# Performance work log

Hardware: AMD Instinct MI355X
Metric: run time of the kernel (lower is better)

## Reference

```python
import jax, jax.numpy as jnp
import numpy as np

E = 1024      # embed_dim
H = 16        # num_heads
HD = E // H   # head_dim = 64
M = 64        # num_landmarks


def setup_inputs() -> dict:
    key = jax.random.key(0)
    ks = jax.random.split(key, 9)
    B, Lq, Lk = 2, 2048, 2048
    inv = 1.0 / np.sqrt(E)
    return {
        "query": jax.random.normal(ks[0], (B, Lq, E), dtype=jnp.float32),
        "key":   jax.random.normal(ks[1], (B, Lk, E), dtype=jnp.float32),
        "value": jax.random.normal(ks[2], (B, Lk, E), dtype=jnp.float32),
        # learned params (xavier-ish scale)
        "Wv": jax.random.normal(ks[3], (E, E), dtype=jnp.float32) * inv,
        "bv": jnp.zeros((E,), dtype=jnp.float32),
        "Wl": jax.random.normal(ks[4], (M, E), dtype=jnp.float32) * inv,
        "bl": jnp.zeros((M,), dtype=jnp.float32),
        "Wo": jax.random.normal(ks[5], (E, E), dtype=jnp.float32) * inv,
        "bo": jnp.zeros((E,), dtype=jnp.float32),
    }


def reference(query, key, value, Wv, bv, Wl, bl, Wo, bo):
    B, Lq, _ = query.shape
    Lk = key.shape[1]
    # value projection -> [B, H, Lk, HD]
    v = (value @ Wv.T + bv).reshape(B, Lk, H, HD).transpose(0, 2, 1, 3)
    # landmark projections + softmax over landmark dim
    ql = jax.nn.softmax((query @ Wl.T + bl) / np.sqrt(M), axis=-1)  # [B, Lq, M]
    kl = jax.nn.softmax((key @ Wl.T + bl) / np.sqrt(M), axis=-1)    # [B, Lk, M]
    # landmark attention: [B, Lq, Lk], scaled by sqrt(head_dim), softmax over keys
    attn = jax.nn.softmax(
        jnp.einsum("bqm,bkm->bqk", ql, kl) / np.sqrt(HD), axis=-1)
    # apply shared attention across heads: [B, H, Lq, HD]
    out_h = jnp.einsum("bqk,bhkd->bhqd", attn, v)
    out = out_h.transpose(0, 2, 1, 3).reshape(B, Lq, E)
    return out @ Wo.T + bo
```

## Files before the change

### kernel.cpp

```cpp
#include <hip/hip_runtime.h>
#include <hip/hip_bf16.h>
#include <cstdint>

typedef unsigned short u16;
typedef __attribute__((ext_vector_type(8))) short short8;
typedef __attribute__((ext_vector_type(4))) float f32x4;
typedef __attribute__((ext_vector_type(4))) unsigned short us4;

__device__ __forceinline__ u16 f2bf(float f) {
    union { float f; unsigned int i; } v; v.f = f;
    unsigned int x = v.i;
    unsigned int r = x + 0x7fffu + ((x >> 16) & 1u);
    return (u16)(r >> 16);
}

enum { EPI_F32 = 0, EPI_BF16 = 1, EPI_EXP_RS = 3, EPI_F32_DIV_CB = 4, EPI_LMSM = 5 };

template <int BM, int BN, int EPI>
__global__ void __launch_bounds__(256)
gemm_bt(const u16* __restrict__ A, const u16* __restrict__ B, void* __restrict__ Cv,
        int M, int N, int K, long sA, long sB, long sC,
        const float* __restrict__ biasCol, float* __restrict__ rowScale, float expScale)
{
    constexpr int BK = 64;
    constexpr int MFRAG = (BM + 31) / 32;
    constexpr int NFRAG = BN / 32;
    __shared__ alignas(16) u16 As[BM * BK];
    __shared__ alignas(16) u16 Bs[BN * BK];

    const int tid = threadIdx.x;
    const int lane = tid & 63;
    const int quad = lane >> 4;
    const int l15 = lane & 15;
    const int w = tid >> 6;
    const int wm = w >> 1, wn = w & 1;
    const int z = blockIdx.z;
    const int m0 = blockIdx.y * BM;
    const int n0 = blockIdx.x * BN;

    const u16* Ab = A + (long)z * sA + (long)m0 * K;
    const u16* Bb = B + (long)z * sB + (long)n0 * K;

    const int r8 = tid >> 3;
    const int cl = tid & 7;
    const int cg = ((cl ^ (r8 & 7)) * 8);

    const u16* ap[(BM + 31) / 32];
#pragma unroll
    for (int j = 0; j < (BM + 31) / 32; ++j) ap[j] = Ab + (long)(j * 32 + r8) * K + cg;
    const u16* bp[BN / 32];
#pragma unroll
    for (int j = 0; j < BN / 32; ++j) bp[j] = Bb + (long)(j * 32 + r8) * K + cg;

    f32x4 acc[MFRAG][NFRAG] = {};

    const int sw = l15 & 7;

    for (int k0 = 0; k0 < K; k0 += BK) {
#pragma unroll
        for (int j = 0; j < (BM + 31) / 32; ++j) {
            __builtin_amdgcn_global_load_lds(
                (const __attribute__((address_space(1))) void*)(ap[j]),
                (__attribute__((address_space(3))) void*)(&As[(j * 32 + r8) * BK + cl * 8]),
                16, 0, 0);
            ap[j] += BK;
        }
#pragma unroll
        for (int j = 0; j < BN / 32; ++j) {
            __builtin_amdgcn_global_load_lds(
                (const __attribute__((address_space(1))) void*)(bp[j]),
                (__attribute__((address_space(3))) void*)(&Bs[(j * 32 + r8) * BK + cl * 8]),
                16, 0, 0);
            bp[j] += BK;
        }
        __syncthreads();
#pragma unroll
        for (int ks = 0; ks < 2; ++ks) {
            short8 af[MFRAG], bfr[NFRAG];
#pragma unroll
            for (int i = 0; i < MFRAG; ++i)
                af[i] = *(const short8*)&As[(wm * (BM / 2) + i * 16 + l15) * BK +
                                            (((ks * 4 + quad) ^ sw) * 8)];
#pragma unroll
            for (int i = 0; i < NFRAG; ++i)
                bfr[i] = *(const short8*)&Bs[(wn * (BN / 2) + i * 16 + l15) * BK +
                                             (((ks * 4 + quad) ^ sw) * 8)];
#pragma unroll
            for (int i = 0; i < MFRAG; ++i)
#pragma unroll
                for (int jn = 0; jn < NFRAG; ++jn)
                    acc[i][jn] = __builtin_amdgcn_mfma_f32_16x16x32_bf16(af[i], bfr[jn], acc[i][jn], 0, 0, 0);
        }
        __syncthreads();
    }

    if constexpr (EPI == EPI_LMSM) {
        __shared__ float red[2][BM];
        float ev[4][NFRAG];
#pragma unroll
        for (int r = 0; r < 4; ++r) {
            float s = 0.f;
#pragma unroll
            for (int jn = 0; jn < NFRAG; ++jn) {
                const int col = wn * (BN / 2) + jn * 16 + l15;
                float v = exp2f((acc[0][jn][r] + biasCol[col]) * expScale);
                ev[r][jn] = v; s += v;
            }
            s += __shfl_xor(s, 1); s += __shfl_xor(s, 2);
            s += __shfl_xor(s, 4); s += __shfl_xor(s, 8);
            if (l15 == 0) red[wn][wm * 16 + quad * 4 + r] = s;
        }
        __syncthreads();
#pragma unroll
        for (int r = 0; r < 4; ++r) {
            const int mrow = wm * 16 + quad * 4 + r;
            const float inv = 1.0f / (red[0][mrow] + red[1][mrow]);
            const long m = m0 + mrow;
#pragma unroll
            for (int jn = 0; jn < NFRAG; ++jn) {
                const int col = wn * (BN / 2) + jn * 16 + l15;
                ((u16*)Cv)[m * N + col] = f2bf(ev[r][jn] * inv);
            }
        }
        return;
    } else {
#pragma unroll
        for (int i = 0; i < MFRAG; ++i) {
            const int mb = m0 + wm * (BM / 2) + i * 16 + quad * 4;
#pragma unroll
            for (int r = 0; r < 4; ++r) {
                const int m = mb + r;
                float rin = 0.f;
                if constexpr (EPI == EPI_F32_DIV_CB) rin = 1.0f / rowScale[(long)z * M + m];
                float rowsum = 0.f;
#pragma unroll
                for (int jn = 0; jn < NFRAG; ++jn) {
                    const int col = n0 + wn * (BN / 2) + jn * 16 + l15;
                    float v = acc[i][jn][r];
                    if constexpr (EPI == EPI_EXP_RS) { v = exp2f(v * expScale); rowsum += v; }
                    if constexpr (EPI == EPI_F32_DIV_CB) v = v * rin + biasCol[col];
                    if constexpr (EPI == EPI_F32 || EPI == EPI_F32_DIV_CB)
                        ((float*)Cv)[(long)z * sC + (long)m * N + col] = v;
                    else
                        ((u16*)Cv)[(long)z * sC + (long)m * N + col] = f2bf(v);
                }
                if constexpr (EPI == EPI_EXP_RS) {
                    rowsum += __shfl_xor(rowsum, 1);
                    rowsum += __shfl_xor(rowsum, 2);
                    rowsum += __shfl_xor(rowsum, 4);
                    rowsum += __shfl_xor(rowsum, 8);
                    if (l15 == 0) atomicAdd(&rowScale[(long)z * M + m], rowsum);
                }
            }
        }
    }
}

__global__ void __launch_bounds__(256)
cast_qkv(const float* __restrict__ a, const float* __restrict__ b, const float* __restrict__ c,
         u16* __restrict__ oa, u16* __restrict__ ob, u16* __restrict__ oc, long n)
{
    const float* s; u16* d;
    if (blockIdx.y == 0)      { s = a; d = oa; }
    else if (blockIdx.y == 1) { s = b; d = ob; }
    else                      { s = c; d = oc; }
    long i = ((long)blockIdx.x * 256 + threadIdx.x) * 4;
    if (i < n) {
        const float4 v = *(const float4*)(s + i);
        us4 o;
        o.x = f2bf(v.x); o.y = f2bf(v.y); o.z = f2bf(v.z); o.w = f2bf(v.w);
        *(us4*)(d + i) = o;
    }
}

__global__ void __launch_bounds__(256)
cast_wowl(const float* __restrict__ wo, const float* __restrict__ wl,
          u16* __restrict__ owo, u16* __restrict__ owl)
{
    long i = ((long)blockIdx.x * 256 + threadIdx.x) * 4;
    const float* s; u16* d;
    if (i < 1048576) { s = wo; d = owo; }
    else { i -= 1048576; s = wl; d = owl; }
    const float4 v = *(const float4*)(s + i);
    us4 o;
    o.x = f2bf(v.x); o.y = f2bf(v.y); o.z = f2bf(v.z); o.w = f2bf(v.w);
    *(us4*)(d + i) = o;
}

__global__ void __launch_bounds__(256)
castT_wv(const float* __restrict__ src, u16* __restrict__ dst, float* __restrict__ rsc)
{
    __shared__ float t[64][65];
    const int bx = blockIdx.x, by = blockIdx.y;
    const int tid = threadIdx.x;
#pragma unroll
    for (int p = 0; p < 16; ++p) {
        int idx = p * 256 + tid;
        int r = idx >> 6, c = idx & 63;
        t[r][c] = src[(long)(by * 64 + r) * 1024 + bx * 64 + c];
    }
    __syncthreads();
#pragma unroll
    for (int p = 0; p < 16; ++p) {
        int idx = p * 256 + tid;
        int c = idx >> 6, r = idx & 63;
        dst[(long)(bx * 64 + c) * 1024 + by * 64 + r] = f2bf(t[r][c]);
    }
    if (bx == 0 && by < 16) rsc[by * 256 + tid] = 0.f;
}

__global__ void __launch_bounds__(256)
bias_comb(const float* __restrict__ Wo, const float* __restrict__ bv,
          const float* __restrict__ bo, float* __restrict__ out)
{
    int row = blockIdx.x * 4 + (threadIdx.x >> 6);
    int lane = threadIdx.x & 63;
    float s = 0.f;
#pragma unroll
    for (int i = 0; i < 16; ++i) s += Wo[(long)row * 1024 + i * 64 + lane] * bv[i * 64 + lane];
    for (int o = 32; o; o >>= 1) s += __shfl_xor(s, o, 64);
    if (lane == 0) out[row] = bo[row] + s;
}

extern "C" void kernel_launch(void* const* d_in, const int* in_sizes, int n_in,
                              void* d_out, int out_size, void* d_ws, size_t ws_size,
                              hipStream_t stream)
{
    const float* query = (const float*)d_in[0];
    const float* key   = (const float*)d_in[1];
    const float* value = (const float*)d_in[2];
    const float* Wv    = (const float*)d_in[3];
    const float* bv    = (const float*)d_in[4];
    const float* Wl    = (const float*)d_in[5];
    const float* bl    = (const float*)d_in[6];
    const float* Wo    = (const float*)d_in[7];
    const float* bo    = (const float*)d_in[8];
    float* out = (float*)d_out;

    char* ws = (char*)d_ws;
    u16*   qkb    = (u16*)  (ws + 0);
    u16*   vb     = (u16*)  (ws + 16777216);
    u16*   Wlb    = (u16*)  (ws + 25165824);
    u16*   Wob    = (u16*)  (ws + 25296896);
    u16*   WvT    = (u16*)  (ws + 27394048);
    u16*   Wov    = (u16*)  (ws + 29491200);
    u16*   qlkl   = (u16*)  (ws + 31588352);
    u16*   Ut     = (u16*)  (ws + 32636928);
    u16*   Pm     = (u16*)  (ws + 41025536);
    float* rsc    = (float*)(ws + 57802752);
    float* bocomb = (float*)(ws + 57819136);

    cast_qkv<<<dim3(4096, 3), 256, 0, stream>>>(query, key, value,
                                                qkb, qkb + 4194304, vb, 4194304);
    cast_wowl<<<dim3(1088), 256, 0, stream>>>(Wo, Wl, Wob, Wlb);
    castT_wv<<<dim3(16, 16), 256, 0, stream>>>(Wv, WvT, rsc);
    bias_comb<<<dim3(256), 256, 0, stream>>>(Wo, bv, bo, bocomb);

    gemm_bt<32, 64, EPI_LMSM><<<dim3(1, 256, 1), 256, 0, stream>>>(
        qkb, Wlb, qlkl, 8192, 64, 1024, 0, 0, 0, bl, nullptr, 0.18033688011112042f);

    gemm_bt<64, 64, EPI_BF16><<<dim3(16, 16, 1), 256, 0, stream>>>(
        Wob, WvT, Wov, 1024, 1024, 1024, 0, 0, 0, nullptr, nullptr, 0.f);

    gemm_bt<128, 64, EPI_BF16><<<dim3(32, 8, 2), 256, 0, stream>>>(
        Wov, vb, Ut, 1024, 2048, 1024, 0, 2097152, 2097152, nullptr, nullptr, 0.f);

    gemm_bt<128, 128, EPI_EXP_RS><<<dim3(16, 16, 2), 256, 0, stream>>>(
        qlkl, qlkl + 262144, Pm, 2048, 2048, 64,
        131072, 131072, 4194304, nullptr, rsc, 0.18033688011112042f);

    gemm_bt<64, 128, EPI_F32_DIV_CB><<<dim3(8, 32, 2), 256, 0, stream>>>(
        Pm, Ut, out, 2048, 1024, 2048,
        4194304, 2097152, 2097152, bocomb, rsc, 0.f);
}
```

Baseline: 201.3 us.

## Fuse fp32-to-bf16 casts of activations into GEMM loads and merge prep kernels

Removes the standalone cast of query, key and value to bf16. The landmark GEMM and the value GEMM now read fp32 directly and convert while staging tiles into LDS. The four small weight-prep kernels are merged into one launch. This drops a full round trip of the activations through memory and several launches. The cost is that the converting loads go through registers synchronously instead of async global-to-LDS copies, and in the value GEMM the same fp32 tiles are re-read and re-converted by many blocks.

```diff
diff --git a/kernel.cpp b/kernel.cpp
--- a/kernel.cpp
+++ b/kernel.cpp
@@ -16,15 +16,18 @@
 
 enum { EPI_F32 = 0, EPI_BF16 = 1, EPI_EXP_RS = 3, EPI_F32_DIV_CB = 4, EPI_LMSM = 5 };
 
-template <int BM, int BN, int EPI>
+template <int BM, int BN, int EPI, bool AF32, bool BF32>
 __global__ void __launch_bounds__(256)
-gemm_bt(const u16* __restrict__ A, const u16* __restrict__ B, void* __restrict__ Cv,
+gemm_bt(const void* __restrict__ Ax, const void* __restrict__ A2x,
+        const void* __restrict__ Bx, void* __restrict__ Cv,
         int M, int N, int K, long sA, long sB, long sC,
         const float* __restrict__ biasCol, float* __restrict__ rowScale, float expScale)
 {
     constexpr int BK = 64;
     constexpr int MFRAG = (BM + 31) / 32;
     constexpr int NFRAG = BN / 32;
+    constexpr int AG = (BM + 31) / 32;
+    constexpr int BG = BN / 32;
     __shared__ alignas(16) u16 As[BM * BK];
     __shared__ alignas(16) u16 Bs[BN * BK];
 
@@ -38,40 +41,88 @@
     const int m0 = blockIdx.y * BM;
     const int n0 = blockIdx.x * BN;
 
-    const u16* Ab = A + (long)z * sA + (long)m0 * K;
-    const u16* Bb = B + (long)z * sB + (long)n0 * K;
-
     const int r8 = tid >> 3;
     const int cl = tid & 7;
     const int cg = ((cl ^ (r8 & 7)) * 8);
 
-    const u16* ap[(BM + 31) / 32];
-#pragma unroll
-    for (int j = 0; j < (BM + 31) / 32; ++j) ap[j] = Ab + (long)(j * 32 + r8) * K + cg;
-    const u16* bp[BN / 32];
-#pragma unroll
-    for (int j = 0; j < BN / 32; ++j) bp[j] = Bb + (long)(j * 32 + r8) * K + cg;
+    const u16* ap[AG];
+    const float* apf[AG];
+    if constexpr (AF32) {
+        const float* base = (const float*)Ax;
+        long mr = m0;
+        if (A2x != nullptr && m0 >= (M >> 1)) { base = (const float*)A2x; mr = m0 - (M >> 1); }
+        const float* Afb = base + (long)z * sA + (long)mr * K;
+#pragma unroll
+        for (int j = 0; j < AG; ++j) apf[j] = Afb + (long)(j * 32 + r8) * K + cg;
+    } else {
+        const u16* Ab = (const u16*)Ax + (long)z * sA + (long)m0 * K;
+#pragma unroll
+        for (int j = 0; j < AG; ++j) ap[j] = Ab + (long)(j * 32 + r8) * K + cg;
+    }
+    const u16* bp[BG];
+    const float* bpf[BG];
+    if constexpr (BF32) {
+        const float* Bfb = (const float*)Bx + (long)z * sB + (long)n0 * K;
+#pragma unroll
+        for (int j = 0; j < BG; ++j) bpf[j] = Bfb + (long)(j * 32 + r8) * K + cg;
+    } else {
+        const u16* Bb = (const u16*)Bx + (long)z * sB + (long)n0 * K;
+#pragma unroll
+        for (int j = 0; j < BG; ++j) bp[j] = Bb + (long)(j * 32 + r8) * K + cg;
+    }
 
     f32x4 acc[MFRAG][NFRAG] = {};
 
     const int sw = l15 & 7;
 
     for (int k0 = 0; k0 < K; k0 += BK) {
-#pragma unroll
-        for (int j = 0; j < (BM + 31) / 32; ++j) {
-            __builtin_amdgcn_global_load_lds(
-                (const __attribute__((address_space(1))) void*)(ap[j]),
-                (__attribute__((address_space(3))) void*)(&As[(j * 32 + r8) * BK + cl * 8]),
-                16, 0, 0);
-            ap[j] += BK;
-        }
-#pragma unroll
-        for (int j = 0; j < BN / 32; ++j) {
-            __builtin_amdgcn_global_load_lds(
-                (const __attribute__((address_space(1))) void*)(bp[j]),
-                (__attribute__((address_space(3))) void*)(&Bs[(j * 32 + r8) * BK + cl * 8]),
-                16, 0, 0);
-            bp[j] += BK;
+        if constexpr (!AF32) {
+#pragma unroll
+            for (int j = 0; j < AG; ++j) {
+                __builtin_amdgcn_global_load_lds(
+                    (const __attribute__((address_space(1))) void*)(ap[j]),
+                    (__attribute__((address_space(3))) void*)(&As[(j * 32 + r8) * BK + cl * 8]),
+                    16, 0, 0);
+                ap[j] += BK;
+            }
+        }
+        if constexpr (!BF32) {
+#pragma unroll
+            for (int j = 0; j < BG; ++j) {
+                __builtin_amdgcn_global_load_lds(
+                    (const __attribute__((address_space(1))) void*)(bp[j]),
+                    (__attribute__((address_space(3))) void*)(&Bs[(j * 32 + r8) * BK + cl * 8]),
+                    16, 0, 0);
+                bp[j] += BK;
+            }
+        }
+        if constexpr (AF32) {
+#pragma unroll
+            for (int j = 0; j < AG; ++j) {
+                const float4 u0 = *(const float4*)(apf[j]);
+                const float4 u1 = *(const float4*)(apf[j] + 4);
+                short8 o;
+                o[0] = (short)f2bf(u0.x); o[1] = (short)f2bf(u0.y);
+                o[2] = (short)f2bf(u0.z); o[3] = (short)f2bf(u0.w);
+                o[4] = (short)f2bf(u1.x); o[5] = (short)f2bf(u1.y);
+                o[6] = (short)f2bf(u1.z); o[7] = (short)f2bf(u1.w);
+                *(short8*)&As[(j * 32 + r8) * BK + cl * 8] = o;
+                apf[j] += BK;
+            }
+        }
+        if constexpr (BF32) {
+#pragma unroll
+            for (int j = 0; j < BG; ++j) {
+                const float4 u0 = *(const float4*)(bpf[j]);
+                const float4 u1 = *(const float4*)(bpf[j] + 4);
+                short8 o;
+                o[0] = (short)f2bf(u0.x); o[1] = (short)f2bf(u0.y);
+                o[2] = (short)f2bf(u0.z); o[3] = (short)f2bf(u0.w);
+                o[4] = (short)f2bf(u1.x); o[5] = (short)f2bf(u1.y);
+                o[6] = (short)f2bf(u1.z); o[7] = (short)f2bf(u1.w);
+                *(short8*)&Bs[(j * 32 + r8) * BK + cl * 8] = o;
+                bpf[j] += BK;
+            }
         }
         __syncthreads();
 #pragma unroll
@@ -157,69 +208,50 @@
 }
 
 __global__ void __launch_bounds__(256)
-cast_qkv(const float* __restrict__ a, const float* __restrict__ b, const float* __restrict__ c,
-         u16* __restrict__ oa, u16* __restrict__ ob, u16* __restrict__ oc, long n)
+prep_all(const float* __restrict__ Wo, const float* __restrict__ Wl,
+         const float* __restrict__ Wv, const float* __restrict__ bv,
+         const float* __restrict__ bo,
+         u16* __restrict__ Wob, u16* __restrict__ Wlb, u16* __restrict__ WvT,
+         float* __restrict__ rsc, float* __restrict__ bocomb)
 {
-    const float* s; u16* d;
-    if (blockIdx.y == 0)      { s = a; d = oa; }
-    else if (blockIdx.y == 1) { s = b; d = ob; }
-    else                      { s = c; d = oc; }
-    long i = ((long)blockIdx.x * 256 + threadIdx.x) * 4;
-    if (i < n) {
+    __shared__ float t[64][65];
+    const int b = blockIdx.x;
+    const int tid = threadIdx.x;
+    if (b < 1088) {
+        long i = ((long)b * 256 + tid) * 4;
+        const float* s; u16* d;
+        if (i < 1048576) { s = Wo; d = Wob; }
+        else { i -= 1048576; s = Wl; d = Wlb; }
         const float4 v = *(const float4*)(s + i);
         us4 o;
         o.x = f2bf(v.x); o.y = f2bf(v.y); o.z = f2bf(v.z); o.w = f2bf(v.w);
         *(us4*)(d + i) = o;
-    }
-}
-
-__global__ void __launch_bounds__(256)
-cast_wowl(const float* __restrict__ wo, const float* __restrict__ wl,
-          u16* __restrict__ owo, u16* __restrict__ owl)
-{
-    long i = ((long)blockIdx.x * 256 + threadIdx.x) * 4;
-    const float* s; u16* d;
-    if (i < 1048576) { s = wo; d = owo; }
-    else { i -= 1048576; s = wl; d = owl; }
-    const float4 v = *(const float4*)(s + i);
-    us4 o;
-    o.x = f2bf(v.x); o.y = f2bf(v.y); o.z = f2bf(v.z); o.w = f2bf(v.w);
-    *(us4*)(d + i) = o;
-}
-
-__global__ void __launch_bounds__(256)
-castT_wv(const float* __restrict__ src, u16* __restrict__ dst, float* __restrict__ rsc)
-{
-    __shared__ float t[64][65];
-    const int bx = blockIdx.x, by = blockIdx.y;
-    const int tid = threadIdx.x;
-#pragma unroll
-    for (int p = 0; p < 16; ++p) {
-        int idx = p * 256 + tid;
-        int r = idx >> 6, c = idx & 63;
-        t[r][c] = src[(long)(by * 64 + r) * 1024 + bx * 64 + c];
-    }
-    __syncthreads();
-#pragma unroll
-    for (int p = 0; p < 16; ++p) {
-        int idx = p * 256 + tid;
-        int c = idx >> 6, r = idx & 63;
-        dst[(long)(bx * 64 + c) * 1024 + by * 64 + r] = f2bf(t[r][c]);
-    }
-    if (bx == 0 && by < 16) rsc[by * 256 + tid] = 0.f;
-}
-
-__global__ void __launch_bounds__(256)
-bias_comb(const float* __restrict__ Wo, const float* __restrict__ bv,
-          const float* __restrict__ bo, float* __restrict__ out)
-{
-    int row = blockIdx.x * 4 + (threadIdx.x >> 6);
-    int lane = threadIdx.x & 63;
-    float s = 0.f;
-#pragma unroll
-    for (int i = 0; i < 16; ++i) s += Wo[(long)row * 1024 + i * 64 + lane] * bv[i * 64 + lane];
-    for (int o = 32; o; o >>= 1) s += __shfl_xor(s, o, 64);
-    if (lane == 0) out[row] = bo[row] + s;
+    } else if (b < 1344) {
+        const int bidx = b - 1088;
+        const int bx = bidx & 15, by = bidx >> 4;
+#pragma unroll
+        for (int p = 0; p < 16; ++p) {
+            int idx = p * 256 + tid;
+            int r = idx >> 6, c = idx & 63;
+            t[r][c] = Wv[(long)(by * 64 + r) * 1024 + bx * 64 + c];
+        }
+        __syncthreads();
+#pragma unroll
+        for (int p = 0; p < 16; ++p) {
+            int idx = p * 256 + tid;
+            int c = idx >> 6, r = idx & 63;
+            WvT[(long)(bx * 64 + c) * 1024 + by * 64 + r] = f2bf(t[r][c]);
+        }
+        if (bx == 0) rsc[by * 256 + tid] = 0.f;
+    } else {
+        const int row = (b - 1344) * 4 + (tid >> 6);
+        const int lane = tid & 63;
+        float s = 0.f;
+#pragma unroll
+        for (int i = 0; i < 16; ++i) s += Wo[(long)row * 1024 + i * 64 + lane] * bv[i * 64 + lane];
+        for (int o = 32; o; o >>= 1) s += __shfl_xor(s, o, 64);
+        if (lane == 0) bocomb[row] = bo[row] + s;
+    }
 }
 
 extern "C" void kernel_launch(void* const* d_in, const int* in_sizes, int n_in,
@@ -238,8 +270,6 @@
     float* out = (float*)d_out;
 
     char* ws = (char*)d_ws;
-    u16*   qkb    = (u16*)  (ws + 0);
-    u16*   vb     = (u16*)  (ws + 16777216);
     u16*   Wlb    = (u16*)  (ws + 25165824);
     u16*   Wob    = (u16*)  (ws + 25296896);
     u16*   WvT    = (u16*)  (ws + 27394048);
@@ -250,26 +280,23 @@
     float* rsc    = (float*)(ws + 57802752);
     float* bocomb = (float*)(ws + 57819136);
 
-    cast_qkv<<<dim3(4096, 3), 256, 0, stream>>>(query, key, value,
-                                                qkb, qkb + 4194304, vb, 4194304);
-    cast_wowl<<<dim3(1088), 256, 0, stream>>>(Wo, Wl, Wob, Wlb);
-    castT_wv<<<dim3(16, 16), 256, 0, stream>>>(Wv, WvT, rsc);
-    bias_comb<<<dim3(256), 256, 0, stream>>>(Wo, bv, bo, bocomb);
-
-    gemm_bt<32, 64, EPI_LMSM><<<dim3(1, 256, 1), 256, 0, stream>>>(
-        qkb, Wlb, qlkl, 8192, 64, 1024, 0, 0, 0, bl, nullptr, 0.18033688011112042f);
-
-    gemm_bt<64, 64, EPI_BF16><<<dim3(16, 16, 1), 256, 0, stream>>>(
-        Wob, WvT, Wov, 1024, 1024, 1024, 0, 0, 0, nullptr, nullptr, 0.f);
-
-    gemm_bt<128, 64, EPI_BF16><<<dim3(32, 8, 2), 256, 0, stream>>>(
-        Wov, vb, Ut, 1024, 2048, 1024, 0, 2097152, 2097152, nullptr, nullptr, 0.f);
-
-    gemm_bt<128, 128, EPI_EXP_RS><<<dim3(16, 16, 2), 256, 0, stream>>>(
-        qlkl, qlkl + 262144, Pm, 2048, 2048, 64,
+    prep_all<<<dim3(1600), 256, 0, stream>>>(Wo, Wl, Wv, bv, bo,
+                                             Wob, Wlb, WvT, rsc, bocomb);
+
+    gemm_bt<32, 64, EPI_LMSM, true, false><<<dim3(1, 256, 1), 256, 0, stream>>>(
+        query, key, Wlb, qlkl, 8192, 64, 1024, 0, 0, 0, bl, nullptr, 0.18033688011112042f);
+
+    gemm_bt<64, 64, EPI_BF16, false, false><<<dim3(16, 16, 1), 256, 0, stream>>>(
+        Wob, nullptr, WvT, Wov, 1024, 1024, 1024, 0, 0, 0, nullptr, nullptr, 0.f);
+
+    gemm_bt<128, 64, EPI_BF16, false, true><<<dim3(32, 8, 2), 256, 0, stream>>>(
+        Wov, nullptr, value, Ut, 1024, 2048, 1024, 0, 2097152, 2097152, nullptr, nullptr, 0.f);
+
+    gemm_bt<128, 128, EPI_EXP_RS, false, false><<<dim3(16, 16, 2), 256, 0, stream>>>(
+        qlkl, nullptr, qlkl + 262144, Pm, 2048, 2048, 64,
         131072, 131072, 4194304, nullptr, rsc, 0.18033688011112042f);
 
-    gemm_bt<64, 128, EPI_F32_DIV_CB><<<dim3(8, 32, 2), 256, 0, stream>>>(
-        Pm, Ut, out, 2048, 1024, 2048,
+    gemm_bt<64, 128, EPI_F32_DIV_CB, false, false><<<dim3(8, 32, 2), 256, 0, stream>>>(
+        Pm, nullptr, Ut, out, 2048, 1024, 2048,
         4194304, 2097152, 2097152, bocomb, rsc, 0.f);
 }
```

After: 194.4 us. 1.04x faster.
